# Kernel optimization log

Hardware: AMD Instinct MI355X
Metric: run time of the kernel (lower is better)

## Reference

```python
import jax, jax.numpy as jnp
import numpy as np

N_NODES = 100000
N_EDGES = 1600000
IN_DIM = 128
OUT_DIM = 64
EDGE_DIM = 8


def setup_inputs() -> dict:
    key = jax.random.key(0)
    ks = jax.random.split(key, 7)
    h = jax.random.normal(ks[0], (N_NODES, IN_DIM), dtype=jnp.float32)
    edge_index = jax.random.randint(ks[1], (2, N_EDGES), 0, N_NODES, dtype=jnp.int64)
    edge_attr = jax.random.normal(ks[2], (N_EDGES, EDGE_DIM), dtype=jnp.float32)
    w_w = jax.random.normal(ks[3], (IN_DIM, OUT_DIM), dtype=jnp.float32) * (1.0 / np.sqrt(IN_DIM))
    w_b = jax.random.normal(ks[4], (OUT_DIM,), dtype=jnp.float32) * 0.01
    a_w = jax.random.normal(ks[5], (2 * OUT_DIM + EDGE_DIM, 1), dtype=jnp.float32) * 0.1
    a_b = jax.random.normal(ks[6], (1,), dtype=jnp.float32) * 0.01
    return {"h": h, "edge_index": edge_index, "edge_attr": edge_attr,
            "w_w": w_w, "w_b": w_b, "a_w": a_w, "a_b": a_b}


def reference(h, edge_index, edge_attr, w_w, w_b, a_w, a_b):
    n = h.shape[0]
    d = w_w.shape[1]
    wh = h @ w_w + w_b                              # [N, out_dim]
    row, col = edge_index[0], edge_index[1]
    # a([wh[row], wh[col], edge_attr]) == wh[row]@a1 + wh[col]@a2 + edge_attr@a3 + b
    a1, a2, a3 = a_w[:d], a_w[d:2 * d], a_w[2 * d:]
    s_row = wh @ a1                                 # [N, 1] per-node attention terms
    s_col = wh @ a2                                 # [N, 1]
    e = jax.nn.leaky_relu(s_row[row] + s_col[col] + edge_attr @ a3 + a_b)  # [E, 1]
    # segment softmax over edges grouped by destination `row`
    max_e = jax.ops.segment_max(e, row, num_segments=n)     # [N, 1]
    alpha = jnp.exp(e - max_e[row])                          # [E, 1]
    out = jax.ops.segment_sum(alpha * wh[col], row, num_segments=n)  # [N, out_dim]
    norm = jax.ops.segment_sum(alpha, row, num_segments=n)           # [N, 1]
    return out / (norm + 1e-8)
```

## Files before the change

kernel.cpp:

```cpp
#include <hip/hip_runtime.h>
#include <hip/hip_fp16.h>

#define IN_DIM 128
#define OUT_DIM 64
#define RPB 128
#define MAXB 800
#define EPB 4096
#define ENTL 2304
#define CAP 3584

typedef __attribute__((ext_vector_type(8))) _Float16 half8;
typedef __attribute__((ext_vector_type(4))) float f32x4;

__global__ __launch_bounds__(256) void k_wh(
    const float* __restrict__ h, const float* __restrict__ w_w,
    const float* __restrict__ w_b, const float* __restrict__ a_w,
    __half* __restrict__ wh, float* __restrict__ s_row,
    float* __restrict__ s_col, int* __restrict__ gcur, int n_nodes) {
  {
    int tid = blockIdx.x * 256 + threadIdx.x;
    if (tid < MAXB) gcur[tid] = 0;
  }
  __shared__ _Float16 wf[4 * 4 * 64 * 8];
  for (int idx = threadIdx.x; idx < IN_DIM * OUT_DIM; idx += 256) {
    int k = idx >> 6, c = idx & 63;
    int mt = c >> 4;
    int kt = k >> 5;
    int l = (((k >> 3) & 3) << 4) | (c & 15);
    int j = k & 7;
    wf[(((mt << 2) | kt) << 9) | (l << 3) | j] = (_Float16)w_w[idx];
  }
  __syncthreads();

  const int lane = threadIdx.x & 63;
  const int wv = threadIdx.x >> 6;

  half8 A[4][4];
#pragma unroll
  for (int mt = 0; mt < 4; ++mt)
#pragma unroll
    for (int kt = 0; kt < 4; ++kt)
      A[mt][kt] =
          *(const half8*)&wf[(((mt << 2) | kt) << 9) | (lane << 3)];

  const int cbase = (lane >> 4) << 2;
  f32x4 bq[4], a1q[4], a2q[4];
#pragma unroll
  for (int mt = 0; mt < 4; ++mt) {
    bq[mt] = *(const f32x4*)&w_b[mt * 16 + cbase];
    a1q[mt] = *(const f32x4*)&a_w[mt * 16 + cbase];
    a2q[mt] = *(const f32x4*)&a_w[OUT_DIM + mt * 16 + cbase];
  }

  const int ntiles = (n_nodes + 15) >> 4;
  const int tstride = gridDim.x << 2;
  for (int t = blockIdx.x * 4 + wv; t < ntiles; t += tstride) {
    const int n0 = t << 4;
    const int node = n0 + (lane & 15);
    const int nodec = node < n_nodes ? node : n_nodes - 1;
    const float4* hv =
        (const float4*)(h + (size_t)nodec * IN_DIM + ((lane >> 4) << 3));
    float4 p[8];
#pragma unroll
    for (int kt = 0; kt < 4; ++kt) {
      p[2 * kt] = hv[kt * 8];
      p[2 * kt + 1] = hv[kt * 8 + 1];
    }
    f32x4 C[4];
#pragma unroll
    for (int mt = 0; mt < 4; ++mt) C[mt] = (f32x4){0.f, 0.f, 0.f, 0.f};
#pragma unroll
    for (int kt = 0; kt < 4; ++kt) {
      const float4 u = p[2 * kt], v = p[2 * kt + 1];
      half8 B;
      B[0] = (_Float16)u.x; B[1] = (_Float16)u.y;
      B[2] = (_Float16)u.z; B[3] = (_Float16)u.w;
      B[4] = (_Float16)v.x; B[5] = (_Float16)v.y;
      B[6] = (_Float16)v.z; B[7] = (_Float16)v.w;
#pragma unroll
      for (int mt = 0; mt < 4; ++mt)
        C[mt] = __builtin_amdgcn_mfma_f32_16x16x32_f16(A[mt][kt], B, C[mt],
                                                       0, 0, 0);
    }
    float sr = 0.f, sc = 0.f;
    uint2 q[4];
#pragma unroll
    for (int mt = 0; mt < 4; ++mt) {
      f32x4 d = C[mt] + bq[mt];
      sr += d[0] * a1q[mt][0] + d[1] * a1q[mt][1] + d[2] * a1q[mt][2] +
            d[3] * a1q[mt][3];
      sc += d[0] * a2q[mt][0] + d[1] * a2q[mt][1] + d[2] * a2q[mt][2] +
            d[3] * a2q[mt][3];
      __half2 lo = __floats2half2_rn(d[0], d[1]);
      __half2 hi = __floats2half2_rn(d[2], d[3]);
      q[mt].x = *(unsigned int*)&lo;
      q[mt].y = *(unsigned int*)&hi;
    }
    if (node < n_nodes) {
      uint2* wrow = (uint2*)(wh + (size_t)node * OUT_DIM + cbase);
      wrow[0] = q[0];
      wrow[4] = q[1];
      wrow[8] = q[2];
      wrow[12] = q[3];
    }
    sr += __shfl_xor(sr, 16, 64);
    sr += __shfl_xor(sr, 32, 64);
    sc += __shfl_xor(sc, 16, 64);
    sc += __shfl_xor(sc, 32, 64);
    if (lane < 16 && node < n_nodes) {
      s_row[node] = sr;
      s_col[node] = sc;
    }
  }
}

__global__ __launch_bounds__(512) void k_fill(
    const int* __restrict__ ei, const float* __restrict__ edge_attr,
    const float* __restrict__ a_w, int* __restrict__ gcur,
    int2* __restrict__ entA, int nedges, int nb) {
  __shared__ int hist[MAXB];
  __shared__ int cbase[MAXB];
  __shared__ int curs[MAXB];
  for (int b = threadIdx.x; b < MAXB; b += 512) hist[b] = 0;
  const float aw0 = a_w[128], aw1 = a_w[129], aw2 = a_w[130], aw3 = a_w[131];
  const float aw4 = a_w[132], aw5 = a_w[133], aw6 = a_w[134], aw7 = a_w[135];
  __syncthreads();
  const int e0 = blockIdx.x * EPB;
  int row[8], col[8];
  float s[8];
#pragma unroll
  for (int k = 0; k < 8; ++k) {
    int e = e0 + k * 512 + threadIdx.x;
    if (e < nedges) {
      row[k] = ei[e];
      col[k] = ei[nedges + e];
    } else {
      row[k] = -1;
      col[k] = 0;
    }
  }
#pragma unroll
  for (int k = 0; k < 8; ++k) {
    int e = e0 + k * 512 + threadIdx.x;
    if (row[k] >= 0) {
      const float4* ea = (const float4*)(edge_attr + (size_t)e * 8);
      float4 u = ea[0], v = ea[1];
      float t = u.x * aw0 + u.y * aw1 + u.z * aw2 + u.w * aw3;
      t += v.x * aw4 + v.y * aw5 + v.z * aw6 + v.w * aw7;
      s[k] = t;
    } else {
      s[k] = 0.f;
    }
  }
#pragma unroll
  for (int k = 0; k < 8; ++k)
    if (row[k] >= 0) atomicAdd(&hist[row[k] >> 7], 1);
  __syncthreads();
  for (int b = threadIdx.x; b < nb; b += 512) {
    int c = hist[b];
    int cb = 0;
    if (c > 0) cb = b * CAP + atomicAdd(&gcur[b], (c + 7) & ~7);
    cbase[b] = cb;
    curs[b] = cb;
  }
  __syncthreads();
#pragma unroll
  for (int k = 0; k < 8; ++k) {
    if (row[k] >= 0) {
      int bb = row[k] >> 7;
      int pos = atomicAdd(&curs[bb], 1);
      entA[pos] = make_int2(((row[k] & 127) << 17) | col[k],
                            __float_as_int(s[k]));
    }
  }
  __syncthreads();
  for (int b = threadIdx.x; b < nb; b += 512) {
    int c = hist[b];
    if (c > 0) {
      int st = cbase[b] + c, end = cbase[b] + ((c + 7) & ~7);
      for (int k = st; k < end; ++k) entA[k] = make_int2(-1, 0);
    }
  }
}

__global__ __launch_bounds__(512) void k_sagg(
    const int2* __restrict__ entA, const int* __restrict__ gcur,
    const __half* __restrict__ wh,
    const float* __restrict__ s_row, const float* __restrict__ s_col,
    const float* __restrict__ a_b, float* __restrict__ out, int n_nodes) {
  __shared__ int2 entl[ENTL];
  __shared__ int hist[RPB], sd[RPB], starts[RPB], curs[RPB], degs[RPB];
  const int b = blockIdx.x;
  const int row0 = b << 7;
  const int t = threadIdx.x;
  if (t < RPB) hist[t] = 0;
  __syncthreads();
  const int c = gcur[b];
  const int base = b * CAP;
  int2 e[8];
#pragma unroll
  for (int k = 0; k < 8; ++k) {
    int i = t + k * 512;
    e[k] = (i < c) ? entA[base + i] : make_int2(-1, 0);
  }
#pragma unroll
  for (int k = 0; k < 8; ++k)
    if (e[k].x >= 0) atomicAdd(&hist[e[k].x >> 17], 1);
  for (int i = t + 4096; i < c; i += 512) {
    int2 p = entA[base + i];
    if (p.x >= 0) atomicAdd(&hist[p.x >> 17], 1);
  }
  __syncthreads();
  int hh = 0;
  if (t < RPB) { hh = hist[t]; sd[t] = hh; }
  __syncthreads();
  for (int off = 1; off < RPB; off <<= 1) {
    int x = (t >= off && t < RPB) ? sd[t - off] : 0;
    __syncthreads();
    if (t < RPB) sd[t] += x;
    __syncthreads();
  }
  if (t < RPB) {
    int excl = sd[t] - hh;
    starts[t] = excl;
    curs[t] = excl;
    degs[t] = hh;
  }
  __syncthreads();
#pragma unroll
  for (int k = 0; k < 8; ++k)
    if (e[k].x >= 0) {
      int p = atomicAdd(&curs[e[k].x >> 17], 1);
      if (p < ENTL) entl[p] = e[k];
    }
  for (int i = t + 4096; i < c; i += 512) {
    int2 p2 = entA[base + i];
    if (p2.x >= 0) {
      int p = atomicAdd(&curs[p2.x >> 17], 1);
      if (p < ENTL) entl[p] = p2;
    }
  }
  __syncthreads();
  const int wv = t >> 6;
  const int lane = t & 63;
  const int slot = lane >> 3, sub = lane & 7;
  const float ab = a_b[0];
  const uint4* whq = (const uint4*)wh;
  for (int j = 0; j < 16; ++j) {
    const int rl = wv * 16 + j;
    const int node = row0 + rl;
    if (node >= n_nodes) break;
    const int st = starts[rl];
    const int dg = degs[rl];
    const float sab = s_row[node] + ab;
    float acc[8] = {0.f, 0.f, 0.f, 0.f, 0.f, 0.f, 0.f, 0.f};
    float l = 0.f;
    for (int bas = 0; bas < dg; bas += 16) {
      const int i0 = bas + slot, i1 = bas + 8 + slot;
      const bool g0 = i0 < dg, g1 = i1 < dg;
      int2 p0 = g0 ? entl[st + i0] : make_int2(0, 0);
      int2 p1 = g1 ? entl[st + i1] : make_int2(0, 0);
      const int col0 = p0.x & 0x1FFFF, col1 = p1.x & 0x1FFFF;
      uint4 q0 = make_uint4(0, 0, 0, 0), q1 = make_uint4(0, 0, 0, 0);
      float sc0 = 0.f, sc1 = 0.f;
      if (g0) { q0 = whq[(size_t)col0 * 8 + sub]; sc0 = s_col[col0]; }
      if (g1) { q1 = whq[(size_t)col1 * 8 + sub]; sc1 = s_col[col1]; }
      if (g0) {
        float s = sab + sc0 + __int_as_float(p0.y);
        float ev = (s > 0.f) ? s : 0.01f * s;
        float a = __expf(ev);
        float2 f0 = __half22float2(*(__half2*)&q0.x);
        float2 f1 = __half22float2(*(__half2*)&q0.y);
        float2 f2 = __half22float2(*(__half2*)&q0.z);
        float2 f3 = __half22float2(*(__half2*)&q0.w);
        acc[0] = fmaf(a, f0.x, acc[0]); acc[1] = fmaf(a, f0.y, acc[1]);
        acc[2] = fmaf(a, f1.x, acc[2]); acc[3] = fmaf(a, f1.y, acc[3]);
        acc[4] = fmaf(a, f2.x, acc[4]); acc[5] = fmaf(a, f2.y, acc[5]);
        acc[6] = fmaf(a, f3.x, acc[6]); acc[7] = fmaf(a, f3.y, acc[7]);
        if (sub == 0) l += a;
      }
      if (g1) {
        float s = sab + sc1 + __int_as_float(p1.y);
        float ev = (s > 0.f) ? s : 0.01f * s;
        float a = __expf(ev);
        float2 f0 = __half22float2(*(__half2*)&q1.x);
        float2 f1 = __half22float2(*(__half2*)&q1.y);
        float2 f2 = __half22float2(*(__half2*)&q1.z);
        float2 f3 = __half22float2(*(__half2*)&q1.w);
        acc[0] = fmaf(a, f0.x, acc[0]); acc[1] = fmaf(a, f0.y, acc[1]);
        acc[2] = fmaf(a, f1.x, acc[2]); acc[3] = fmaf(a, f1.y, acc[3]);
        acc[4] = fmaf(a, f2.x, acc[4]); acc[5] = fmaf(a, f2.y, acc[5]);
        acc[6] = fmaf(a, f3.x, acc[6]); acc[7] = fmaf(a, f3.y, acc[7]);
        if (sub == 0) l += a;
      }
    }
#pragma unroll
    for (int d = 0; d < 8; ++d) {
      acc[d] += __shfl_xor(acc[d], 8, 64);
      acc[d] += __shfl_xor(acc[d], 16, 64);
      acc[d] += __shfl_xor(acc[d], 32, 64);
    }
    l += __shfl_xor(l, 8, 64);
    l += __shfl_xor(l, 16, 64);
    l += __shfl_xor(l, 32, 64);
    float lt = __shfl(l, 0, 64);
    if (slot == 0) {
      float inv = 1.0f / (lt + 1e-8f);
      float4 o0 = make_float4(acc[0] * inv, acc[1] * inv, acc[2] * inv,
                              acc[3] * inv);
      float4 o1 = make_float4(acc[4] * inv, acc[5] * inv, acc[6] * inv,
                              acc[7] * inv);
      float4* orow = (float4*)out + (size_t)node * 16 + sub * 2;
      orow[0] = o0;
      orow[1] = o1;
    }
  }
}

extern "C" void kernel_launch(void* const* d_in, const int* in_sizes, int n_in,
                              void* d_out, int out_size, void* d_ws, size_t ws_size,
                              hipStream_t stream) {
  const float* h         = (const float*)d_in[0];
  const int*   ei        = (const int*)d_in[1];
  const float* edge_attr = (const float*)d_in[2];
  const float* w_w       = (const float*)d_in[3];
  const float* w_b       = (const float*)d_in[4];
  const float* a_w       = (const float*)d_in[5];
  const float* a_b       = (const float*)d_in[6];
  const int n_nodes = in_sizes[0] / IN_DIM;
  const int nedges  = in_sizes[1] / 2;
  const int nb   = (n_nodes + RPB - 1) / RPB;
  const int nebl = (nedges + EPB - 1) / EPB;

  __half* wh       = (__half*)d_ws;
  int2*  entA      = (int2*)(wh + (size_t)n_nodes * OUT_DIM);
  int*   gcur      = (int*)(entA + (size_t)nb * CAP);
  float* s_row     = (float*)(gcur + MAXB);
  float* s_col     = s_row + n_nodes;

  k_wh<<<640, 256, 0, stream>>>(h, w_w, w_b, a_w, wh, s_row, s_col, gcur,
                                n_nodes);
  k_fill<<<nebl, 512, 0, stream>>>(ei, edge_attr, a_w, gcur, entA,
                                   nedges, nb);
  k_sagg<<<nb, 512, 0, stream>>>(entA, gcur, wh, s_row, s_col, a_b,
                                 (float*)d_out, n_nodes);
}
```

Baseline: 234.9 us.

## Merge node transform and edge bucketing into one concurrent kernel

The dense wh/score kernel and the edge bucketing kernel are independent, so they are merged into one launch. Blocks below nfill do edge bucketing and the remaining NWH blocks do the MFMA node transform. The aim is to overlap the two memory-bound phases and drop one dependent launch boundary. Zeroing gcur moves into a tiny separate kernel, which adds a launch, and the merged kernel's LDS use is the union of both branches, which may lower occupancy.

```diff
diff --git a/kernel.cpp b/kernel.cpp
--- a/kernel.cpp
+++ b/kernel.cpp
@@ -8,177 +8,178 @@
 #define EPB 4096
 #define ENTL 2304
 #define CAP 3584
+#define NWH 320
 
 typedef __attribute__((ext_vector_type(8))) _Float16 half8;
 typedef __attribute__((ext_vector_type(4))) float f32x4;
 
-__global__ __launch_bounds__(256) void k_wh(
+__global__ __launch_bounds__(256) void k_zero(int* __restrict__ gcur) {
+  for (int i = threadIdx.x; i < MAXB; i += 256) gcur[i] = 0;
+}
+
+__global__ __launch_bounds__(512) void k_whfill(
     const float* __restrict__ h, const float* __restrict__ w_w,
     const float* __restrict__ w_b, const float* __restrict__ a_w,
+    const int* __restrict__ ei, const float* __restrict__ edge_attr,
     __half* __restrict__ wh, float* __restrict__ s_row,
-    float* __restrict__ s_col, int* __restrict__ gcur, int n_nodes) {
-  {
-    int tid = blockIdx.x * 256 + threadIdx.x;
-    if (tid < MAXB) gcur[tid] = 0;
-  }
-  __shared__ _Float16 wf[4 * 4 * 64 * 8];
-  for (int idx = threadIdx.x; idx < IN_DIM * OUT_DIM; idx += 256) {
-    int k = idx >> 6, c = idx & 63;
-    int mt = c >> 4;
-    int kt = k >> 5;
-    int l = (((k >> 3) & 3) << 4) | (c & 15);
-    int j = k & 7;
-    wf[(((mt << 2) | kt) << 9) | (l << 3) | j] = (_Float16)w_w[idx];
-  }
-  __syncthreads();
-
-  const int lane = threadIdx.x & 63;
-  const int wv = threadIdx.x >> 6;
-
-  half8 A[4][4];
-#pragma unroll
-  for (int mt = 0; mt < 4; ++mt)
-#pragma unroll
-    for (int kt = 0; kt < 4; ++kt)
-      A[mt][kt] =
-          *(const half8*)&wf[(((mt << 2) | kt) << 9) | (lane << 3)];
-
-  const int cbase = (lane >> 4) << 2;
-  f32x4 bq[4], a1q[4], a2q[4];
-#pragma unroll
-  for (int mt = 0; mt < 4; ++mt) {
-    bq[mt] = *(const f32x4*)&w_b[mt * 16 + cbase];
-    a1q[mt] = *(const f32x4*)&a_w[mt * 16 + cbase];
-    a2q[mt] = *(const f32x4*)&a_w[OUT_DIM + mt * 16 + cbase];
-  }
-
-  const int ntiles = (n_nodes + 15) >> 4;
-  const int tstride = gridDim.x << 2;
-  for (int t = blockIdx.x * 4 + wv; t < ntiles; t += tstride) {
-    const int n0 = t << 4;
-    const int node = n0 + (lane & 15);
-    const int nodec = node < n_nodes ? node : n_nodes - 1;
-    const float4* hv =
-        (const float4*)(h + (size_t)nodec * IN_DIM + ((lane >> 4) << 3));
-    float4 p[8];
-#pragma unroll
-    for (int kt = 0; kt < 4; ++kt) {
-      p[2 * kt] = hv[kt * 8];
-      p[2 * kt + 1] = hv[kt * 8 + 1];
-    }
-    f32x4 C[4];
-#pragma unroll
-    for (int mt = 0; mt < 4; ++mt) C[mt] = (f32x4){0.f, 0.f, 0.f, 0.f};
-#pragma unroll
-    for (int kt = 0; kt < 4; ++kt) {
-      const float4 u = p[2 * kt], v = p[2 * kt + 1];
-      half8 B;
-      B[0] = (_Float16)u.x; B[1] = (_Float16)u.y;
-      B[2] = (_Float16)u.z; B[3] = (_Float16)u.w;
-      B[4] = (_Float16)v.x; B[5] = (_Float16)v.y;
-      B[6] = (_Float16)v.z; B[7] = (_Float16)v.w;
-#pragma unroll
-      for (int mt = 0; mt < 4; ++mt)
-        C[mt] = __builtin_amdgcn_mfma_f32_16x16x32_f16(A[mt][kt], B, C[mt],
-                                                       0, 0, 0);
-    }
-    float sr = 0.f, sc = 0.f;
-    uint2 q[4];
+    float* __restrict__ s_col, int* __restrict__ gcur,
+    int2* __restrict__ entA, int n_nodes, int nedges, int nb, int nfill) {
+  if ((int)blockIdx.x < nfill) {
+    __shared__ int hist[MAXB];
+    __shared__ int cbase[MAXB];
+    __shared__ int curs[MAXB];
+    for (int b = threadIdx.x; b < MAXB; b += 512) hist[b] = 0;
+    const float aw0 = a_w[128], aw1 = a_w[129], aw2 = a_w[130], aw3 = a_w[131];
+    const float aw4 = a_w[132], aw5 = a_w[133], aw6 = a_w[134], aw7 = a_w[135];
+    __syncthreads();
+    const int e0 = blockIdx.x * EPB;
+    int row[8], col[8];
+    float s[8];
+#pragma unroll
+    for (int k = 0; k < 8; ++k) {
+      int e = e0 + k * 512 + threadIdx.x;
+      if (e < nedges) {
+        row[k] = ei[e];
+        col[k] = ei[nedges + e];
+      } else {
+        row[k] = -1;
+        col[k] = 0;
+      }
+    }
+#pragma unroll
+    for (int k = 0; k < 8; ++k) {
+      int e = e0 + k * 512 + threadIdx.x;
+      if (row[k] >= 0) {
+        const float4* ea = (const float4*)(edge_attr + (size_t)e * 8);
+        float4 u = ea[0], v = ea[1];
+        float t = u.x * aw0 + u.y * aw1 + u.z * aw2 + u.w * aw3;
+        t += v.x * aw4 + v.y * aw5 + v.z * aw6 + v.w * aw7;
+        s[k] = t;
+      } else {
+        s[k] = 0.f;
+      }
+    }
+#pragma unroll
+    for (int k = 0; k < 8; ++k)
+      if (row[k] >= 0) atomicAdd(&hist[row[k] >> 7], 1);
+    __syncthreads();
+    for (int b = threadIdx.x; b < nb; b += 512) {
+      int c = hist[b];
+      int cb = 0;
+      if (c > 0) cb = b * CAP + atomicAdd(&gcur[b], (c + 7) & ~7);
+      cbase[b] = cb;
+      curs[b] = cb;
+    }
+    __syncthreads();
+#pragma unroll
+    for (int k = 0; k < 8; ++k) {
+      if (row[k] >= 0) {
+        int bb = row[k] >> 7;
+        int pos = atomicAdd(&curs[bb], 1);
+        entA[pos] = make_int2(((row[k] & 127) << 17) | col[k],
+                              __float_as_int(s[k]));
+      }
+    }
+    __syncthreads();
+    for (int b = threadIdx.x; b < nb; b += 512) {
+      int c = hist[b];
+      if (c > 0) {
+        int st = cbase[b] + c, end = cbase[b] + ((c + 7) & ~7);
+        for (int k = st; k < end; ++k) entA[k] = make_int2(-1, 0);
+      }
+    }
+  } else {
+    __shared__ _Float16 wf[4 * 4 * 64 * 8];
+    for (int idx = threadIdx.x; idx < IN_DIM * OUT_DIM; idx += 512) {
+      int k = idx >> 6, c = idx & 63;
+      int mt = c >> 4;
+      int kt = k >> 5;
+      int l = (((k >> 3) & 3) << 4) | (c & 15);
+      int j = k & 7;
+      wf[(((mt << 2) | kt) << 9) | (l << 3) | j] = (_Float16)w_w[idx];
+    }
+    __syncthreads();
+
+    const int lane = threadIdx.x & 63;
+    const int wv = threadIdx.x >> 6;
+
+    half8 A[4][4];
+#pragma unroll
+    for (int mt = 0; mt < 4; ++mt)
+#pragma unroll
+      for (int kt = 0; kt < 4; ++kt)
+        A[mt][kt] =
+            *(const half8*)&wf[(((mt << 2) | kt) << 9) | (lane << 3)];
+
+    const int cbase2 = (lane >> 4) << 2;
+    f32x4 bq[4], a1q[4], a2q[4];
 #pragma unroll
     for (int mt = 0; mt < 4; ++mt) {
-      f32x4 d = C[mt] + bq[mt];
-      sr += d[0] * a1q[mt][0] + d[1] * a1q[mt][1] + d[2] * a1q[mt][2] +
-            d[3] * a1q[mt][3];
-      sc += d[0] * a2q[mt][0] + d[1] * a2q[mt][1] + d[2] * a2q[mt][2] +
-            d[3] * a2q[mt][3];
-      __half2 lo = __floats2half2_rn(d[0], d[1]);
-      __half2 hi = __floats2half2_rn(d[2], d[3]);
-      q[mt].x = *(unsigned int*)&lo;
-      q[mt].y = *(unsigned int*)&hi;
-    }
-    if (node < n_nodes) {
-      uint2* wrow = (uint2*)(wh + (size_t)node * OUT_DIM + cbase);
-      wrow[0] = q[0];
-      wrow[4] = q[1];
-      wrow[8] = q[2];
-      wrow[12] = q[3];
-    }
-    sr += __shfl_xor(sr, 16, 64);
-    sr += __shfl_xor(sr, 32, 64);
-    sc += __shfl_xor(sc, 16, 64);
-    sc += __shfl_xor(sc, 32, 64);
-    if (lane < 16 && node < n_nodes) {
-      s_row[node] = sr;
-      s_col[node] = sc;
-    }
-  }
-}
-
-__global__ __launch_bounds__(512) void k_fill(
-    const int* __restrict__ ei, const float* __restrict__ edge_attr,
-    const float* __restrict__ a_w, int* __restrict__ gcur,
-    int2* __restrict__ entA, int nedges, int nb) {
-  __shared__ int hist[MAXB];
-  __shared__ int cbase[MAXB];
-  __shared__ int curs[MAXB];
-  for (int b = threadIdx.x; b < MAXB; b += 512) hist[b] = 0;
-  const float aw0 = a_w[128], aw1 = a_w[129], aw2 = a_w[130], aw3 = a_w[131];
-  const float aw4 = a_w[132], aw5 = a_w[133], aw6 = a_w[134], aw7 = a_w[135];
-  __syncthreads();
-  const int e0 = blockIdx.x * EPB;
-  int row[8], col[8];
-  float s[8];
-#pragma unroll
-  for (int k = 0; k < 8; ++k) {
-    int e = e0 + k * 512 + threadIdx.x;
-    if (e < nedges) {
-      row[k] = ei[e];
-      col[k] = ei[nedges + e];
-    } else {
-      row[k] = -1;
-      col[k] = 0;
-    }
-  }
-#pragma unroll
-  for (int k = 0; k < 8; ++k) {
-    int e = e0 + k * 512 + threadIdx.x;
-    if (row[k] >= 0) {
-      const float4* ea = (const float4*)(edge_attr + (size_t)e * 8);
-      float4 u = ea[0], v = ea[1];
-      float t = u.x * aw0 + u.y * aw1 + u.z * aw2 + u.w * aw3;
-      t += v.x * aw4 + v.y * aw5 + v.z * aw6 + v.w * aw7;
-      s[k] = t;
-    } else {
-      s[k] = 0.f;
-    }
-  }
-#pragma unroll
-  for (int k = 0; k < 8; ++k)
-    if (row[k] >= 0) atomicAdd(&hist[row[k] >> 7], 1);
-  __syncthreads();
-  for (int b = threadIdx.x; b < nb; b += 512) {
-    int c = hist[b];
-    int cb = 0;
-    if (c > 0) cb = b * CAP + atomicAdd(&gcur[b], (c + 7) & ~7);
-    cbase[b] = cb;
-    curs[b] = cb;
-  }
-  __syncthreads();
-#pragma unroll
-  for (int k = 0; k < 8; ++k) {
-    if (row[k] >= 0) {
-      int bb = row[k] >> 7;
-      int pos = atomicAdd(&curs[bb], 1);
-      entA[pos] = make_int2(((row[k] & 127) << 17) | col[k],
-                            __float_as_int(s[k]));
-    }
-  }
-  __syncthreads();
-  for (int b = threadIdx.x; b < nb; b += 512) {
-    int c = hist[b];
-    if (c > 0) {
-      int st = cbase[b] + c, end = cbase[b] + ((c + 7) & ~7);
-      for (int k = st; k < end; ++k) entA[k] = make_int2(-1, 0);
+      bq[mt] = *(const f32x4*)&w_b[mt * 16 + cbase2];
+      a1q[mt] = *(const f32x4*)&a_w[mt * 16 + cbase2];
+      a2q[mt] = *(const f32x4*)&a_w[OUT_DIM + mt * 16 + cbase2];
+    }
+
+    const int wb = blockIdx.x - nfill;
+    const int ntiles = (n_nodes + 15) >> 4;
+    const int tstride = NWH * 8;
+    for (int t = wb * 8 + wv; t < ntiles; t += tstride) {
+      const int n0 = t << 4;
+      const int node = n0 + (lane & 15);
+      const int nodec = node < n_nodes ? node : n_nodes - 1;
+      const float4* hv =
+          (const float4*)(h + (size_t)nodec * IN_DIM + ((lane >> 4) << 3));
+      float4 p[8];
+#pragma unroll
+      for (int kt = 0; kt < 4; ++kt) {
+        p[2 * kt] = hv[kt * 8];
+        p[2 * kt + 1] = hv[kt * 8 + 1];
+      }
+      f32x4 C[4];
+#pragma unroll
+      for (int mt = 0; mt < 4; ++mt) C[mt] = (f32x4){0.f, 0.f, 0.f, 0.f};
+#pragma unroll
+      for (int kt = 0; kt < 4; ++kt) {
+        const float4 u = p[2 * kt], v = p[2 * kt + 1];
+        half8 B;
+        B[0] = (_Float16)u.x; B[1] = (_Float16)u.y;
+        B[2] = (_Float16)u.z; B[3] = (_Float16)u.w;
+        B[4] = (_Float16)v.x; B[5] = (_Float16)v.y;
+        B[6] = (_Float16)v.z; B[7] = (_Float16)v.w;
+#pragma unroll
+        for (int mt = 0; mt < 4; ++mt)
+          C[mt] = __builtin_amdgcn_mfma_f32_16x16x32_f16(A[mt][kt], B, C[mt],
+                                                         0, 0, 0);
+      }
+      float sr = 0.f, sc = 0.f;
+      uint2 q[4];
+#pragma unroll
+      for (int mt = 0; mt < 4; ++mt) {
+        f32x4 d = C[mt] + bq[mt];
+        sr += d[0] * a1q[mt][0] + d[1] * a1q[mt][1] + d[2] * a1q[mt][2] +
+              d[3] * a1q[mt][3];
+        sc += d[0] * a2q[mt][0] + d[1] * a2q[mt][1] + d[2] * a2q[mt][2] +
+              d[3] * a2q[mt][3];
+        __half2 lo = __floats2half2_rn(d[0], d[1]);
+        __half2 hi = __floats2half2_rn(d[2], d[3]);
+        q[mt].x = *(unsigned int*)&lo;
+        q[mt].y = *(unsigned int*)&hi;
+      }
+      if (node < n_nodes) {
+        uint2* wrow = (uint2*)(wh + (size_t)node * OUT_DIM + cbase2);
+        wrow[0] = q[0];
+        wrow[4] = q[1];
+        wrow[8] = q[2];
+        wrow[12] = q[3];
+      }
+      sr += __shfl_xor(sr, 16, 64);
+      sr += __shfl_xor(sr, 32, 64);
+      sc += __shfl_xor(sc, 16, 64);
+      sc += __shfl_xor(sc, 32, 64);
+      if (lane < 16 && node < n_nodes) {
+        s_row[node] = sr;
+        s_col[node] = sc;
+      }
     }
   }
 }
@@ -338,10 +339,10 @@
   float* s_row     = (float*)(gcur + MAXB);
   float* s_col     = s_row + n_nodes;
 
-  k_wh<<<640, 256, 0, stream>>>(h, w_w, w_b, a_w, wh, s_row, s_col, gcur,
-                                n_nodes);
-  k_fill<<<nebl, 512, 0, stream>>>(ei, edge_attr, a_w, gcur, entA,
-                                   nedges, nb);
+  k_zero<<<1, 256, 0, stream>>>(gcur);
+  k_whfill<<<nebl + NWH, 512, 0, stream>>>(h, w_w, w_b, a_w, ei, edge_attr,
+                                           wh, s_row, s_col, gcur, entA,
+                                           n_nodes, nedges, nb, nebl);
   k_sagg<<<nb, 512, 0, stream>>>(entA, gcur, wh, s_row, s_col, a_b,
                                  (float*)d_out, n_nodes);
 }
```

New measurement: 223.8 us. 4.7% less time.
